# Kernel tuning notes

Measured on AMD Instinct MI355X. Metric: run time of the kernel, lower is better.

## Reference

```python
import jax, jax.numpy as jnp
import numpy as np

B, T, C = 2, 2048, 512
H = 16
HS = C // H  # 32
DF = 4 * C   # 2048
EPS = 1e-3   # keras LayerNormalization default


def setup_inputs() -> dict:
    key = jax.random.key(0)
    ks = jax.random.split(key, 16)
    s = 0.02
    return {
        "x":  jax.random.normal(ks[0], (B, T, C), jnp.float32),
        "Wq": jax.random.normal(ks[1], (H, C, HS), jnp.float32) * s,
        "bq": jnp.zeros((H, HS), jnp.float32),
        "Wk": jax.random.normal(ks[2], (H, C, HS), jnp.float32) * s,
        "bk": jnp.zeros((H, HS), jnp.float32),
        "Wv": jax.random.normal(ks[3], (H, C, HS), jnp.float32) * s,
        "bv": jnp.zeros((H, HS), jnp.float32),
        "Wo": jax.random.normal(ks[4], (C, C), jnp.float32) * s,
        "bo": jnp.zeros((C,), jnp.float32),
        "W1": jax.random.normal(ks[5], (C, DF), jnp.float32) * s,
        "b1": jnp.zeros((DF,), jnp.float32),
        "W2": jax.random.normal(ks[6], (DF, C), jnp.float32) * s,
        "b2": jnp.zeros((C,), jnp.float32),
        "g1": jnp.ones((C,), jnp.float32),
        "be1": jnp.zeros((C,), jnp.float32),
        "g2": jnp.ones((C,), jnp.float32),
        "be2": jnp.zeros((C,), jnp.float32),
    }


def _layernorm(x, g, b):
    mu = jnp.mean(x, axis=-1, keepdims=True)
    var = jnp.mean(jnp.square(x - mu), axis=-1, keepdims=True)
    return (x - mu) / jnp.sqrt(var + EPS) * g + b


def reference(x, Wq, bq, Wk, bk, Wv, bv, Wo, bo, W1, b1, W2, b2, g1, be1, g2, be2):
    Bx, Tx, Cx = x.shape
    # --- attention branch (pre-LN) ---
    h = _layernorm(x, g1, be1)
    q = jnp.einsum('btc,hcd->bhtd', h, Wq) + bq[None, :, None, :]
    k = jnp.einsum('btc,hcd->bhtd', h, Wk) + bk[None, :, None, :]
    v = jnp.einsum('btc,hcd->bhtd', h, Wv) + bv[None, :, None, :]
    # NOTE: source code never applies 1/sqrt(head_size) to scores (mask-only scaling bug)
    scores = jnp.einsum('bhtd,bhsd->bhts', q, k)           # [B,H,T,T]
    causal = jnp.tril(jnp.ones((Tx, Tx), dtype=bool))
    scores = jnp.where(causal, scores, -jnp.inf)
    att = jax.nn.softmax(scores, axis=-1)
    o = jnp.einsum('bhts,bhsd->bhtd', att, v)              # [B,H,T,HS]
    o = o.transpose(0, 2, 1, 3).reshape(Bx, Tx, Cx)        # concat heads
    x = x + o @ Wo + bo
    # --- FFN branch (pre-LN) ---
    h2 = _layernorm(x, g2, be2)
    f = jax.nn.relu(h2 @ W1 + b1) @ W2 + b2
    return x + f
```

## Files before the change

kernel.cpp:

```cpp
#include <hip/hip_runtime.h>
#include <hip/hip_bf16.h>

#define T_  2048
#define C_  512
#define H_  16
#define HS_ 32
#define DF_ 2048
#define B_  2
#define M_  4096

typedef __attribute__((ext_vector_type(8))) short short8;
typedef __attribute__((ext_vector_type(4))) short short4v;
typedef __attribute__((ext_vector_type(4))) float f32x4;
typedef __attribute__((ext_vector_type(16))) float f32x16;

__device__ inline short bf16r(float f) {
  union { float f; unsigned u; } v; v.f = f;
  return (short)((v.u + 0x7FFFu + ((v.u >> 16) & 1u)) >> 16);
}

__device__ inline f32x4 mfma16(short8 a, short8 b, f32x4 c) {
  return __builtin_amdgcn_mfma_f32_16x16x32_bf16(a, b, c, 0, 0, 0);
}
__device__ inline f32x16 mfma32(short8 a, short8 b, f32x16 c) {
  return __builtin_amdgcn_mfma_f32_32x32x16_bf16(a, b, c, 0, 0, 0);
}

__device__ inline unsigned cvtpk(float lo, float hi) {
  unsigned r;
  asm("v_cvt_pk_bf16_f32 %0, %1, %2" : "=v"(r) : "v"(lo), "v"(hi));
  return r;
}

__device__ inline void gload_lds16(const short* g, short* l) {
  __builtin_amdgcn_global_load_lds(
      (const __attribute__((address_space(1))) unsigned int*)g,
      (__attribute__((address_space(3))) unsigned int*)l, 16, 0, 0);
}

__device__ inline void ln_row(int row, const float* src, const float* g,
                              const float* be, short* dst, int lane) {
  const float* xr = src + (size_t)row * C_;
  float4 a = *(const float4*)(xr + lane * 8);
  float4 b = *(const float4*)(xr + lane * 8 + 4);
  float vals[8] = {a.x, a.y, a.z, a.w, b.x, b.y, b.z, b.w};
  float s = 0.f, ss = 0.f;
  #pragma unroll
  for (int i = 0; i < 8; ++i) { s += vals[i]; ss += vals[i] * vals[i]; }
  #pragma unroll
  for (int off = 1; off < 64; off <<= 1) {
    s += __shfl_xor(s, off);
    ss += __shfl_xor(ss, off);
  }
  float mu = s * (1.f / C_);
  float rstd = rsqrtf(ss * (1.f / C_) - mu * mu + 1e-3f);
  short8 o;
  #pragma unroll
  for (int i = 0; i < 8; ++i)
    o[i] = bf16r((vals[i] - mu) * rstd * g[lane * 8 + i] + be[lane * 8 + i]);
  *(short8*)(dst + (size_t)row * C_ + lane * 8) = o;
}

__global__ __launch_bounds__(256) void prep_kernel(
    const float* __restrict__ x, const float* __restrict__ g1, const float* __restrict__ be1,
    const float* __restrict__ Wq, const float* __restrict__ Wk, const float* __restrict__ Wv,
    const float* __restrict__ Wo, const float* __restrict__ W1, const float* __restrict__ W2,
    short* __restrict__ h1, short* __restrict__ Wqkv, short* __restrict__ Wop,
    short* __restrict__ W1p, short* __restrict__ W2p) {
  __shared__ float tile[32][33];
  int id = blockIdx.x;
  int tid = threadIdx.x;
  if (id >= 3072) {
    int w = tid >> 6, lane = tid & 63;
    ln_row((id - 3072) * 4 + w, x, g1, be1, h1, lane);
    return;
  }
  const float* src; short* dst;
  int srcN, dstK, k0, n0;
  size_t dstBase;
  if (id < 768) {
    int s = id >> 4, ct = id & 15;
    int proj = s >> 4, hh = s & 15;
    src = (proj == 0 ? Wq : (proj == 1 ? Wk : Wv)) + (size_t)hh * 512 * 32;
    srcN = 32; dstK = 512; k0 = ct * 32; n0 = 0;
    dst = Wqkv; dstBase = (size_t)(proj * 512 + hh * 32);
  } else if (id < 1024) {
    int t = id - 768;
    src = Wo; srcN = 512; dstK = 512;
    k0 = (t >> 4) * 32; n0 = (t & 15) * 32; dst = Wop; dstBase = 0;
  } else if (id < 2048) {
    int t = id - 1024;
    src = W1; srcN = 2048; dstK = 512;
    k0 = (t >> 6) * 32; n0 = (t & 63) * 32; dst = W1p; dstBase = 0;
  } else {
    int t = id - 2048;
    src = W2; srcN = 512; dstK = 2048;
    k0 = (t >> 4) * 32; n0 = (t & 15) * 32; dst = W2p; dstBase = 0;
  }
  int rr = tid >> 3, rc = (tid & 7) * 4;
  float4 v4 = *(const float4*)(src + (size_t)(k0 + rr) * srcN + n0 + rc);
  tile[rr][rc + 0] = v4.x; tile[rr][rc + 1] = v4.y;
  tile[rr][rc + 2] = v4.z; tile[rr][rc + 3] = v4.w;
  __syncthreads();
  int wn = tid >> 3, wk = (tid & 7) * 4;
  short4v o;
  o[0] = bf16r(tile[wk + 0][wn]);
  o[1] = bf16r(tile[wk + 1][wn]);
  o[2] = bf16r(tile[wk + 2][wn]);
  o[3] = bf16r(tile[wk + 3][wn]);
  *(short4v*)(dst + (dstBase + n0 + wn) * (size_t)dstK + k0 + wk) = o;
}

__global__ __launch_bounds__(256) void ln2_kernel(
    const float* __restrict__ x, const float* __restrict__ g, const float* __restrict__ be,
    short* __restrict__ out) {
  int w = threadIdx.x >> 6, lane = threadIdx.x & 63;
  ln_row(blockIdx.x * 4 + w, x, g, be, out, lane);
}

template<int BM, int BN, int WM, int WN, int KDIM, int FM, int FN>
__device__ inline void gemm_core(const short* __restrict__ A, const short* __restrict__ Bw,
                                 int m0, int n0, f32x4 (&acc)[FM][FN]) {
  static_assert(WM * WN == 4 && FM == BM / WM / 16 && FN == BN / WN / 16, "geometry");
  __shared__ short lA[2][BM * 64];
  __shared__ short lB[2][BN * 64];
  const int tid = threadIdx.x, w = tid >> 6, lane = tid & 63;
  const int cl = lane & 15, g = lane >> 4;
  const int wm = w / WN, wn = w % WN;
  const int srow = tid >> 3;
  const int sug  = (tid & 7) ^ (srow & 7);
  constexpr int NT = KDIM / 64;

  auto stage = [&](int buf, int k0) {
    #pragma unroll
    for (int j = 0; j < BM / 32; ++j)
      gload_lds16(A + (size_t)(m0 + j * 32 + srow) * KDIM + k0 + sug * 8,
                  &lA[buf][j * 2048 + tid * 8]);
    #pragma unroll
    for (int j = 0; j < BN / 32; ++j)
      gload_lds16(Bw + (size_t)(n0 + j * 32 + srow) * KDIM + k0 + sug * 8,
                  &lB[buf][j * 2048 + tid * 8]);
  };

  stage(0, 0);
  __syncthreads();
  int cur = 0;
  for (int t = 0; t < NT; ++t) {
    if (t + 1 < NT) stage(cur ^ 1, (t + 1) * 64);
    #pragma unroll
    for (int kk = 0; kk < 2; ++kk) {
      const int uswz = ((kk * 4 + g) ^ (cl & 7)) * 8;
      short8 a[FM], b[FN];
      #pragma unroll
      for (int mi = 0; mi < FM; ++mi)
        a[mi] = *(const short8*)&lA[cur][(wm * (BM / WM) + mi * 16 + cl) * 64 + uswz];
      #pragma unroll
      for (int ni = 0; ni < FN; ++ni)
        b[ni] = *(const short8*)&lB[cur][(wn * (BN / WN) + ni * 16 + cl) * 64 + uswz];
      #pragma unroll
      for (int mi = 0; mi < FM; ++mi)
        #pragma unroll
        for (int ni = 0; ni < FN; ++ni)
          acc[mi][ni] = mfma16(a[mi], b[ni], acc[mi][ni]);
    }
    __syncthreads();
    cur ^= 1;
  }
}

__global__ __launch_bounds__(256) void gemm_qkvt(
    const short* __restrict__ h1, const short* __restrict__ Wqkv,
    const float* __restrict__ bq, const float* __restrict__ bk,
    const float* __restrict__ bv,
    short* __restrict__ qb, short* __restrict__ kb, short* __restrict__ vTb) {
  int id = blockIdx.x;
  const short *Ap, *Bp;
  int m0, n0;
  bool isv = id >= 256;
  if (!isv) { m0 = (id >> 3) * 128; n0 = (id & 7) * 128; Ap = h1; Bp = Wqkv; }
  else { int t = id - 256; m0 = (t & 3) * 128; n0 = (t >> 2) * 128;
         Ap = Wqkv + 1024 * 512; Bp = h1; }
  f32x4 acc[4][4] = {};
  gemm_core<128, 128, 2, 2, 512, 4, 4>(Ap, Bp, m0, n0, acc);
  int w = threadIdx.x >> 6, lane = threadIdx.x & 63;
  int cl = lane & 15, rb = (lane >> 4) * 4;
  int wm = w >> 1, wn = w & 1;
  if (!isv) {
    #pragma unroll
    for (int mi = 0; mi < 4; ++mi)
      #pragma unroll
      for (int ni = 0; ni < 4; ++ni)
        #pragma unroll
        for (int r = 0; r < 4; ++r) {
          int mm = m0 + wm * 64 + mi * 16 + rb + r;
          int n  = n0 + wn * 64 + ni * 16 + cl;
          int proj = n >> 9, rem = n & 511;
          int hh = rem >> 5, d = rem & 31;
          int b = mm >> 11, t = mm & (T_ - 1);
          size_t bh = (size_t)b * H_ + hh;
          float val = acc[mi][ni][r];
          if (proj == 0) qb[(bh * T_ + t) * HS_ + d] = bf16r(val + bq[rem]);
          else           kb[(bh * T_ + t) * HS_ + d] = bf16r(val + bk[rem]);
        }
  } else {
    #pragma unroll
    for (int mi = 0; mi < 4; ++mi)
      #pragma unroll
      for (int ni = 0; ni < 4; ++ni)
        #pragma unroll
        for (int r = 0; r < 4; ++r) {
          int m = m0 + wm * 64 + mi * 16 + rb + r;
          int n = n0 + wn * 64 + ni * 16 + cl;
          vTb[(size_t)(n >> 11) * (512 * 2048) + (size_t)m * T_ + (n & 2047)] =
              bf16r(acc[mi][ni][r] + bv[m]);
        }
  }
}

__global__ __launch_bounds__(256) void gemm_out(
    const short* __restrict__ A, const short* __restrict__ W,
    const float* __restrict__ bo, const float* __restrict__ xres,
    float* __restrict__ x1) {
  int m0 = blockIdx.x * 64, n0 = blockIdx.y * 64;
  f32x4 acc[2][2] = {};
  gemm_core<64, 64, 2, 2, 512, 2, 2>(A, W, m0, n0, acc);
  int w = threadIdx.x >> 6, lane = threadIdx.x & 63;
  int cl = lane & 15, rb = (lane >> 4) * 4;
  int wm = w >> 1, wn = w & 1;
  #pragma unroll
  for (int mi = 0; mi < 2; ++mi)
    #pragma unroll
    for (int ni = 0; ni < 2; ++ni)
      #pragma unroll
      for (int r = 0; r < 4; ++r) {
        int mm = m0 + wm * 32 + mi * 16 + rb + r;
        int n  = n0 + wn * 32 + ni * 16 + cl;
        x1[(size_t)mm * C_ + n] = acc[mi][ni][r] + bo[n] + xres[(size_t)mm * C_ + n];
      }
}

__global__ __launch_bounds__(256) void gemm_ffn1(
    const short* __restrict__ A, const short* __restrict__ W,
    const float* __restrict__ b1, short* __restrict__ f1) {
  int m0 = blockIdx.x * 128, n0 = blockIdx.y * 128;
  f32x4 acc[4][4] = {};
  gemm_core<128, 128, 2, 2, 512, 4, 4>(A, W, m0, n0, acc);
  int w = threadIdx.x >> 6, lane = threadIdx.x & 63;
  int cl = lane & 15, rb = (lane >> 4) * 4;
  int wm = w >> 1, wn = w & 1;
  #pragma unroll
  for (int mi = 0; mi < 4; ++mi)
    #pragma unroll
    for (int ni = 0; ni < 4; ++ni)
      #pragma unroll
      for (int r = 0; r < 4; ++r) {
        int mm = m0 + wm * 64 + mi * 16 + rb + r;
        int n  = n0 + wn * 64 + ni * 16 + cl;
        f1[(size_t)mm * DF_ + n] = bf16r(fmaxf(acc[mi][ni][r] + b1[n], 0.f));
      }
}

__global__ __launch_bounds__(256) void gemm_ffn2(
    const short* __restrict__ A, const short* __restrict__ W,
    const float* __restrict__ b2, const float* __restrict__ x1,
    float* __restrict__ out) {
  int m0 = blockIdx.x * 64, n0 = blockIdx.y * 64;
  f32x4 acc[2][2] = {};
  gemm_core<64, 64, 2, 2, 2048, 2, 2>(A, W, m0, n0, acc);
  int w = threadIdx.x >> 6, lane = threadIdx.x & 63;
  int cl = lane & 15, rb = (lane >> 4) * 4;
  int wm = w >> 1, wn = w & 1;
  #pragma unroll
  for (int mi = 0; mi < 2; ++mi)
    #pragma unroll
    for (int ni = 0; ni < 2; ++ni)
      #pragma unroll
      for (int r = 0; r < 4; ++r) {
        int mm = m0 + wm * 32 + mi * 16 + rb + r;
        int n  = n0 + wn * 32 + ni * 16 + cl;
        out[(size_t)mm * C_ + n] = acc[mi][ni][r] + b2[n] + x1[(size_t)mm * C_ + n];
      }
}

__global__ __launch_bounds__(256) void attn_kernel(
    const short* __restrict__ qb, const short* __restrict__ kb,
    const short* __restrict__ vTb, short* __restrict__ ob) {
  __shared__ float accbuf[4][64][17];
  __shared__ float lbuf[4][32];
  __shared__ short tbuf[32][34];
  const int id = blockIdx.x;
  const int xcd = id & 7, s = id >> 3;
  const int headin = s & 3;
  const int qt = 63 - (s >> 2);
  const int bh = xcd * 4 + headin;
  const int w = threadIdx.x >> 6, lane = threadIdx.x & 63;
  const int cl = lane & 31, g = lane >> 5;
  const int q0 = qt * 32, q = q0 + cl;
  const float L2E = 1.44269504f;
  const float NFM = -16.f * L2E;

  const short* Qp  = qb  + (size_t)bh * T_ * HS_;
  const short* Kp  = kb  + (size_t)bh * T_ * HS_;
  const short* VTp = vTb + (size_t)bh * HS_ * T_;

  const int nc   = qt + 1;
  const int cbeg = (nc * w) >> 2;
  const int cend = (nc * (w + 1)) >> 2;

  f32x16 acc = {};
  float l = 0.f;

  if (cbeg < cend) {
    short8 qf0 = *(const short8*)(Qp + (size_t)q * HS_ + g * 8);
    short8 qf1 = *(const short8*)(Qp + (size_t)q * HS_ + 16 + g * 8);
    const int kc0 = cbeg << 5;
    short8 ka  = *(const short8*)(Kp + (size_t)(kc0 + cl) * HS_ + g * 8);
    short8 kc2 = *(const short8*)(Kp + (size_t)(kc0 + cl) * HS_ + 16 + g * 8);
    short8 va  = *(const short8*)(VTp + (size_t)cl * T_ + kc0 + g * 8);
    short8 vb  = *(const short8*)(VTp + (size_t)cl * T_ + kc0 + 16 + g * 8);

    for (int c = cbeg; c < cend; ++c) {
      const int kc = c << 5;
      f32x16 Z = {};
      f32x16 S = mfma32(ka, qf0, Z);
      S = mfma32(kc2, qf1, S);

      short8 kan, kbn, van, vbn;
      if (c + 1 < cend) {
        const int kn = kc + 32;
        kan = *(const short8*)(Kp + (size_t)(kn + cl) * HS_ + g * 8);
        kbn = *(const short8*)(Kp + (size_t)(kn + cl) * HS_ + 16 + g * 8);
        van = *(const short8*)(VTp + (size_t)cl * T_ + kn + g * 8);
        vbn = *(const short8*)(VTp + (size_t)cl * T_ + kn + 16 + g * 8);
      }

      if (c == nc - 1) {
        #pragma unroll
        for (int r = 0; r < 16; ++r) {
          int key = kc + (r & 3) + 8 * (r >> 2) + 4 * g;
          if (key > q) S[r] = -1e30f;
        }
      }

      float p[16];
      #pragma unroll
      for (int r = 0; r < 16; ++r) p[r] = exp2f(fmaf(S[r], L2E, NFM));
      float sm[8];
      #pragma unroll
      for (int r = 0; r < 8; ++r) sm[r] = p[r] + p[r + 8];
      #pragma unroll
      for (int r = 0; r < 4; ++r) sm[r] += sm[r + 4];
      float ps = (sm[0] + sm[1]) + (sm[2] + sm[3]);
      ps += __shfl_xor(ps, 32);
      l += ps;

      #pragma unroll
      for (int sb = 0; sb < 2; ++sb) {
        unsigned L0 = cvtpk(p[sb * 8 + 0], p[sb * 8 + 1]);
        unsigned L1 = cvtpk(p[sb * 8 + 2], p[sb * 8 + 3]);
        unsigned H0 = cvtpk(p[sb * 8 + 4], p[sb * 8 + 5]);
        unsigned H1 = cvtpk(p[sb * 8 + 6], p[sb * 8 + 7]);
        auto r02 = __builtin_amdgcn_permlane32_swap(L0, H0, false, false);
        auto r13 = __builtin_amdgcn_permlane32_swap(L1, H1, false, false);
        union { unsigned u[4]; short8 v; } pb;
        pb.u[0] = r02[0]; pb.u[1] = r13[0]; pb.u[2] = r02[1]; pb.u[3] = r13[1];
        acc = mfma32(sb == 0 ? va : vb, pb.v, acc);
      }

      ka = kan; kc2 = kbn; va = van; vb = vbn;
    }
  }

  #pragma unroll
  for (int r = 0; r < 16; ++r) accbuf[w][lane][r] = acc[r];
  if (lane < 32) lbuf[w][cl] = l;
  __syncthreads();

  if (w == 0) {
    float lsum = lbuf[0][cl] + lbuf[1][cl] + lbuf[2][cl] + lbuf[3][cl];
    float inv = 1.f / lsum;
    #pragma unroll
    for (int r = 0; r < 16; ++r) {
      float v = accbuf[0][lane][r] + accbuf[1][lane][r] +
                accbuf[2][lane][r] + accbuf[3][lane][r];
      int d = (r & 3) + 8 * (r >> 2) + 4 * g;
      tbuf[cl][d] = bf16r(v * inv);
    }
  }
  __syncthreads();

  int qr = threadIdx.x >> 3, col = (threadIdx.x & 7) * 4;
  const int b = bh >> 4, hh = bh & 15;
  short4v o4;
  o4[0] = tbuf[qr][col + 0];
  o4[1] = tbuf[qr][col + 1];
  o4[2] = tbuf[qr][col + 2];
  o4[3] = tbuf[qr][col + 3];
  *(short4v*)(ob + ((size_t)b * T_ + q0 + qr) * C_ + hh * HS_ + col) = o4;
}

#define OFF_H1   ((size_t)0)
#define OFF_WQKV ((size_t)4194304)
#define OFF_WO   ((size_t)5767168)
#define OFF_W1   ((size_t)6291456)
#define OFF_W2   ((size_t)8388608)
#define OFF_Q    ((size_t)10485760)
#define OFF_K    ((size_t)14680064)
#define OFF_VT   ((size_t)18874368)
#define OFF_O    ((size_t)23068672)
#define OFF_X1   ((size_t)27262976)
#define OFF_H2   ((size_t)35651584)
#define OFF_F1   ((size_t)39845888)

extern "C" void kernel_launch(void* const* d_in, const int* in_sizes, int n_in,
                              void* d_out, int out_size, void* d_ws, size_t ws_size,
                              hipStream_t stream) {
  const float* x   = (const float*)d_in[0];
  const float* Wq  = (const float*)d_in[1];
  const float* bq  = (const float*)d_in[2];
  const float* Wk  = (const float*)d_in[3];
  const float* bk  = (const float*)d_in[4];
  const float* Wv  = (const float*)d_in[5];
  const float* bv  = (const float*)d_in[6];
  const float* Wo  = (const float*)d_in[7];
  const float* bo  = (const float*)d_in[8];
  const float* W1  = (const float*)d_in[9];
  const float* b1  = (const float*)d_in[10];
  const float* W2  = (const float*)d_in[11];
  const float* b2  = (const float*)d_in[12];
  const float* g1  = (const float*)d_in[13];
  const float* be1 = (const float*)d_in[14];
  const float* g2  = (const float*)d_in[15];
  const float* be2 = (const float*)d_in[16];

  char* ws = (char*)d_ws;
  short* h1   = (short*)(ws + OFF_H1);
  short* Wqkv = (short*)(ws + OFF_WQKV);
  short* Wop  = (short*)(ws + OFF_WO);
  short* W1p  = (short*)(ws + OFF_W1);
  short* W2p  = (short*)(ws + OFF_W2);
  short* qb   = (short*)(ws + OFF_Q);
  short* kb   = (short*)(ws + OFF_K);
  short* vTb  = (short*)(ws + OFF_VT);
  short* ob   = (short*)(ws + OFF_O);
  float* x1   = (float*)(ws + OFF_X1);
  short* h2   = (short*)(ws + OFF_H2);
  short* f1   = (short*)(ws + OFF_F1);
  float* out  = (float*)d_out;

  prep_kernel<<<3072 + 1024, 256, 0, stream>>>(x, g1, be1, Wq, Wk, Wv, Wo, W1, W2,
                                               h1, Wqkv, Wop, W1p, W2p);
  gemm_qkvt<<<384, 256, 0, stream>>>(h1, Wqkv, bq, bk, bv, qb, kb, vTb);
  attn_kernel<<<2048, 256, 0, stream>>>(qb, kb, vTb, ob);
  gemm_out<<<dim3(M_ / 64, C_ / 64), 256, 0, stream>>>(ob, Wop, bo, x, x1);
  ln2_kernel<<<M_ / 4, 256, 0, stream>>>(x1, g2, be2, h2);
  gemm_ffn1<<<dim3(M_ / 128, DF_ / 128), 256, 0, stream>>>(h2, W1p, b1, f1);
  gemm_ffn2<<<dim3(M_ / 64, C_ / 64), 256, 0, stream>>>(f1, W2p, b2, x1, out);
}
```

Baseline: 109.3 us.

## Use 512-thread blocks with intra-block split-K for FFN2 and attention

The FFN2 GEMM now runs 8 waves per block, with two groups of four splitting each 64-wide K tile, double-buffered swizzled LDS staging and an LDS reduction of the partial accumulators. The attention kernel likewise splits each query tile's key chunks over 8 waves instead of 4 and spreads the final reduction across all threads. Both aim to raise per-block parallelism and latency hiding for these small-tile kernels. In exchange they add LDS use, an extra reduction pass and barrier, and finer per-wave work that can leave waves with little or no work on short causal rows.

After: 111.0 us. About the same (+1.5%).

```diff
diff --git a/kernel.cpp b/kernel.cpp
--- a/kernel.cpp
+++ b/kernel.cpp
@@ -260,33 +260,77 @@
       }
 }
 
-__global__ __launch_bounds__(256) void gemm_ffn2(
+__global__ __launch_bounds__(512) void gemm_ffn2(
     const short* __restrict__ A, const short* __restrict__ W,
     const float* __restrict__ b2, const float* __restrict__ x1,
     float* __restrict__ out) {
-  int m0 = blockIdx.x * 64, n0 = blockIdx.y * 64;
+  __shared__ short lA[2][64 * 64];
+  __shared__ short lB[2][64 * 64];
+  __shared__ float accbuf[4][64][17];
+  const int m0 = blockIdx.x * 64, n0 = blockIdx.y * 64;
+  const int tid = threadIdx.x, w = tid >> 6, lane = tid & 63;
+  const int cl = lane & 15, g = lane >> 4;
+  const int q = w & 3, ks = w >> 2;
+  const int wm = q >> 1, wn = q & 1;
+  const int srow = tid >> 3;
+  const int sug  = (tid & 7) ^ (srow & 7);
+  constexpr int NT = 32;
   f32x4 acc[2][2] = {};
-  gemm_core<64, 64, 2, 2, 2048, 2, 2>(A, W, m0, n0, acc);
-  int w = threadIdx.x >> 6, lane = threadIdx.x & 63;
-  int cl = lane & 15, rb = (lane >> 4) * 4;
-  int wm = w >> 1, wn = w & 1;
-  #pragma unroll
-  for (int mi = 0; mi < 2; ++mi)
-    #pragma unroll
-    for (int ni = 0; ni < 2; ++ni)
-      #pragma unroll
-      for (int r = 0; r < 4; ++r) {
-        int mm = m0 + wm * 32 + mi * 16 + rb + r;
-        int n  = n0 + wn * 32 + ni * 16 + cl;
-        out[(size_t)mm * C_ + n] = acc[mi][ni][r] + b2[n] + x1[(size_t)mm * C_ + n];
-      }
-}
-
-__global__ __launch_bounds__(256) void attn_kernel(
+
+  auto stage = [&](int buf, int k0) {
+    gload_lds16(A + (size_t)(m0 + srow) * DF_ + k0 + sug * 8, &lA[buf][tid * 8]);
+    gload_lds16(W + (size_t)(n0 + srow) * DF_ + k0 + sug * 8, &lB[buf][tid * 8]);
+  };
+
+  stage(0, 0);
+  __syncthreads();
+  int cur = 0;
+  for (int t = 0; t < NT; ++t) {
+    if (t + 1 < NT) stage(cur ^ 1, (t + 1) * 64);
+    const int uswz = ((ks * 4 + g) ^ (cl & 7)) * 8;
+    short8 a0 = *(const short8*)&lA[cur][(wm * 32 + cl) * 64 + uswz];
+    short8 a1 = *(const short8*)&lA[cur][(wm * 32 + 16 + cl) * 64 + uswz];
+    short8 b0 = *(const short8*)&lB[cur][(wn * 32 + cl) * 64 + uswz];
+    short8 b1 = *(const short8*)&lB[cur][(wn * 32 + 16 + cl) * 64 + uswz];
+    acc[0][0] = mfma16(a0, b0, acc[0][0]);
+    acc[0][1] = mfma16(a0, b1, acc[0][1]);
+    acc[1][0] = mfma16(a1, b0, acc[1][0]);
+    acc[1][1] = mfma16(a1, b1, acc[1][1]);
+    __syncthreads();
+    cur ^= 1;
+  }
+
+  if (ks == 1) {
+    #pragma unroll
+    for (int mi = 0; mi < 2; ++mi)
+      #pragma unroll
+      for (int ni = 0; ni < 2; ++ni)
+        #pragma unroll
+        for (int r = 0; r < 4; ++r)
+          accbuf[q][lane][mi * 8 + ni * 4 + r] = acc[mi][ni][r];
+  }
+  __syncthreads();
+  if (ks == 0) {
+    int rb = (lane >> 4) * 4;
+    #pragma unroll
+    for (int mi = 0; mi < 2; ++mi)
+      #pragma unroll
+      for (int ni = 0; ni < 2; ++ni)
+        #pragma unroll
+        for (int r = 0; r < 4; ++r) {
+          float v = acc[mi][ni][r] + accbuf[q][lane][mi * 8 + ni * 4 + r];
+          int mm = m0 + wm * 32 + mi * 16 + rb + r;
+          int n  = n0 + wn * 32 + ni * 16 + cl;
+          out[(size_t)mm * C_ + n] = v + b2[n] + x1[(size_t)mm * C_ + n];
+        }
+  }
+}
+
+__global__ __launch_bounds__(512) void attn_kernel(
     const short* __restrict__ qb, const short* __restrict__ kb,
     const short* __restrict__ vTb, short* __restrict__ ob) {
-  __shared__ float accbuf[4][64][17];
-  __shared__ float lbuf[4][32];
+  __shared__ float accbuf[8][64][17];
+  __shared__ float lbuf[8][32];
   __shared__ short tbuf[32][34];
   const int id = blockIdx.x;
   const int xcd = id & 7, s = id >> 3;
@@ -304,8 +348,8 @@
   const short* VTp = vTb + (size_t)bh * HS_ * T_;
 
   const int nc   = qt + 1;
-  const int cbeg = (nc * w) >> 2;
-  const int cend = (nc * (w + 1)) >> 2;
+  const int cbeg = (nc * w) >> 3;
+  const int cend = (nc * (w + 1)) >> 3;
 
   f32x16 acc = {};
   float l = 0.f;
@@ -376,27 +420,32 @@
   if (lane < 32) lbuf[w][cl] = l;
   __syncthreads();
 
-  if (w == 0) {
-    float lsum = lbuf[0][cl] + lbuf[1][cl] + lbuf[2][cl] + lbuf[3][cl];
-    float inv = 1.f / lsum;
-    #pragma unroll
-    for (int r = 0; r < 16; ++r) {
-      float v = accbuf[0][lane][r] + accbuf[1][lane][r] +
-                accbuf[2][lane][r] + accbuf[3][lane][r];
-      int d = (r & 3) + 8 * (r >> 2) + 4 * g;
-      tbuf[cl][d] = bf16r(v * inv);
+  #pragma unroll
+  for (int i = 0; i < 2; ++i) {
+    int e = threadIdx.x * 2 + i;
+    int el = e >> 4, er = e & 15;
+    int eq = el & 31, eg = el >> 5;
+    float v = 0.f, ls = 0.f;
+    #pragma unroll
+    for (int ww = 0; ww < 8; ++ww) {
+      v += accbuf[ww][el][er];
+      ls += lbuf[ww][eq];
     }
+    int d = (er & 3) + 8 * (er >> 2) + 4 * eg;
+    tbuf[eq][d] = bf16r(v / ls);
   }
   __syncthreads();
 
-  int qr = threadIdx.x >> 3, col = (threadIdx.x & 7) * 4;
-  const int b = bh >> 4, hh = bh & 15;
-  short4v o4;
-  o4[0] = tbuf[qr][col + 0];
-  o4[1] = tbuf[qr][col + 1];
-  o4[2] = tbuf[qr][col + 2];
-  o4[3] = tbuf[qr][col + 3];
-  *(short4v*)(ob + ((size_t)b * T_ + q0 + qr) * C_ + hh * HS_ + col) = o4;
+  if (threadIdx.x < 256) {
+    int qr = threadIdx.x >> 3, col = (threadIdx.x & 7) * 4;
+    const int b = bh >> 4, hh = bh & 15;
+    short4v o4;
+    o4[0] = tbuf[qr][col + 0];
+    o4[1] = tbuf[qr][col + 1];
+    o4[2] = tbuf[qr][col + 2];
+    o4[3] = tbuf[qr][col + 3];
+    *(short4v*)(ob + ((size_t)b * T_ + q0 + qr) * C_ + hh * HS_ + col) = o4;
+  }
 }
 
 #define OFF_H1   ((size_t)0)
@@ -451,9 +500,9 @@
   prep_kernel<<<3072 + 1024, 256, 0, stream>>>(x, g1, be1, Wq, Wk, Wv, Wo, W1, W2,
                                                h1, Wqkv, Wop, W1p, W2p);
   gemm_qkvt<<<384, 256, 0, stream>>>(h1, Wqkv, bq, bk, bv, qb, kb, vTb);
-  attn_kernel<<<2048, 256, 0, stream>>>(qb, kb, vTb, ob);
+  attn_kernel<<<2048, 512, 0, stream>>>(qb, kb, vTb, ob);
   gemm_out<<<dim3(M_ / 64, C_ / 64), 256, 0, stream>>>(ob, Wop, bo, x, x1);
   ln2_kernel<<<M_ / 4, 256, 0, stream>>>(x1, g2, be2, h2);
   gemm_ffn1<<<dim3(M_ / 128, DF_ / 128), 256, 0, stream>>>(h2, W1p, b1, f1);
-  gemm_ffn2<<<dim3(M_ / 64, C_ / 64), 256, 0, stream>>>(f1, W2p, b2, x1, out);
-}
+  gemm_ffn2<<<dim3(M_ / 64, C_ / 64), 512, 0, stream>>>(f1, W2p, b2, x1, out);
+}
```
